# Optimization experiments

Hardware: AMD Instinct MI355X
Metric: run time of the kernel (lower is better)

Reference implementation:

```python
import jax, jax.numpy as jnp
import numpy as np

B, S, D, F, H, R, BLK = 1, 2048, 1024, 2816, 16, 16, 64
DH = D // H  # 64

# bitsandbytes NF4 codebook
NF4_CODE = jnp.array([-1.0, -0.6961928009986877, -0.5250730514526367, -0.39491748809814453,
                      -0.28444138169288635, -0.18477343022823334, -0.09105003625154495, 0.0,
                      0.07958029955625534, 0.16093020141124725, 0.24611230194568634, 0.33791524171829224,
                      0.44070982933044434, 0.5626170039176941, 0.7229568362236023, 1.0], dtype=jnp.float32)


def dequant_nf4(codes, absmax, shape):
    # blockwise NF4 dequant: codebook lookup * per-64-element absmax scale
    w = NF4_CODE[codes.reshape(-1)]
    return (w.reshape(-1, BLK) * absmax[:, None]).reshape(shape)


def rmsnorm(x, w, eps=1e-10):
    return x * jax.lax.rsqrt(jnp.mean(x * x, axis=-1, keepdims=True) + eps) * w


def rotate_half(x):
    x1, x2 = jnp.split(x, 2, axis=-1)
    return jnp.concatenate((-x2, x1), axis=-1)


def apply_rope(x, cos, sin, pos):
    # x: [B,H,S,DH], pos: [B,S] -> gather rope tables per position
    c = cos[pos][:, None]  # [B,1,S,DH]
    s = sin[pos][:, None]
    return x * c + rotate_half(x) * s


def proj(x, codes, absmax, la, lb, shape):
    # fused NF4 dequant-matmul + additive LoRA branch: x @ W.T + (x @ A) @ B
    w = dequant_nf4(codes, absmax, shape)
    return x @ w.T + (x @ la) @ lb


def _forward(x, nw1, nw2, cos, sin,
             qa, qla, qlb, ka, kla, klb, va, vla, vlb, oa, ola, olb,
             ga, gla, glb, ua, ula, ulb, da, dla, dlb,
             pos, qc, kc, vc, oc, gc, uc, dc):
    h1 = rmsnorm(x, nw1)
    q = proj(h1, qc, qa, qla, qlb, (D, D))
    k = proj(h1, kc, ka, kla, klb, (D, D))
    v = proj(h1, vc, va, vla, vlb, (D, D))

    def heads(t):
        return t.reshape(B, S, H, DH).transpose(0, 2, 1, 3)

    q = apply_rope(heads(q), cos, sin, pos)
    k = apply_rope(heads(k), cos, sin, pos)
    v = heads(v)

    scores = jnp.einsum('bhqd,bhkd->bhqk', q, k) / np.float32(np.sqrt(DH))
    causal = jnp.tril(jnp.ones((S, S), dtype=bool))
    mask = jnp.where(causal, 0.0, -1e9).astype(scores.dtype)  # additive attention_mask
    attn = jax.nn.softmax(scores + mask, axis=-1)
    o = jnp.einsum('bhqk,bhkd->bhqd', attn, v).transpose(0, 2, 1, 3).reshape(B, S, D)
    o = proj(o, oc, oa, ola, olb, (D, D))

    x1 = x + o  # first residual
    h2 = rmsnorm(x1, nw2)
    gate = proj(h2, gc, ga, gla, glb, (F, D))
    up = proj(h2, uc, ua, ula, ulb, (F, D))
    had = up * jax.nn.silu(gate)  # SwiGLU hadamard
    down = proj(had, dc, da, dla, dlb, (D, F))
    return x1 + down


def setup_inputs():
    ks = iter(jax.random.split(jax.random.key(0), 48))

    def rn(shape, scale=1.0):
        return jax.random.normal(next(ks), shape, jnp.float32) * scale

    def cd(shape):
        return jax.random.randint(next(ks), shape, 0, 16, dtype=jnp.int32)

    def am(n):
        return jax.random.uniform(next(ks), (n,), jnp.float32) * 0.04 + 0.01

    inp = {'x': rn((B, S, D)),
           'norm_weight_1': 1.0 + rn((D,), 0.02),
           'norm_weight_2': 1.0 + rn((D,), 0.02)}
    inv = 1.0 / (10000.0 ** (jnp.arange(0, DH, 2, dtype=jnp.float32) / DH))
    ang = jnp.arange(S, dtype=jnp.float32)[:, None] * inv[None, :]
    emb = jnp.concatenate((ang, ang), axis=-1)  # [S, DH]
    inp['cos'], inp['sin'] = jnp.cos(emb), jnp.sin(emb)
    inp['position_ids'] = jnp.broadcast_to(jnp.arange(S, dtype=jnp.int32), (B, S))
    shapes = {'q': (D, D), 'k': (D, D), 'v': (D, D), 'o': (D, D),
              'gate': (F, D), 'up': (F, D), 'down': (D, F)}
    for p, (o, i) in shapes.items():
        inp['w_%s_codes' % p] = cd((o, i))
        inp['w_%s_absmax' % p] = am(o * i // BLK)
        inp['w_%s_lora_a' % p] = rn((i, R), 1.0 / np.sqrt(i))
        inp['w_%s_lora_b' % p] = rn((R, o), 0.01)
    return inp


def reference(x, norm_weight_1, norm_weight_2, cos, sin, position_ids,
              w_q_codes, w_q_absmax, w_q_lora_a, w_q_lora_b,
              w_k_codes, w_k_absmax, w_k_lora_a, w_k_lora_b,
              w_v_codes, w_v_absmax, w_v_lora_a, w_v_lora_b,
              w_o_codes, w_o_absmax, w_o_lora_a, w_o_lora_b,
              w_gate_codes, w_gate_absmax, w_gate_lora_a, w_gate_lora_b,
              w_up_codes, w_up_absmax, w_up_lora_a, w_up_lora_b,
              w_down_codes, w_down_absmax, w_down_lora_a, w_down_lora_b):
    return _forward(x, norm_weight_1, norm_weight_2, cos, sin,
                    w_q_absmax, w_q_lora_a, w_q_lora_b,
                    w_k_absmax, w_k_lora_a, w_k_lora_b,
                    w_v_absmax, w_v_lora_a, w_v_lora_b,
                    w_o_absmax, w_o_lora_a, w_o_lora_b,
                    w_gate_absmax, w_gate_lora_a, w_gate_lora_b,
                    w_up_absmax, w_up_lora_a, w_up_lora_b,
                    w_down_absmax, w_down_lora_a, w_down_lora_b,
                    position_ids, w_q_codes, w_k_codes, w_v_codes,
                    w_o_codes, w_gate_codes, w_up_codes, w_down_codes)
```

## Files before the change

### kernel.cpp

```cpp
#include <hip/hip_runtime.h>
#include <stdint.h>


#define Sq   2048
#define Dm   1024
#define Fm   2816
#define Hh   16
#define KE1  1088
#define KE2  1056
#define KE3  2848
#define NQKV 3072
#define NGU  5632

typedef short bf16x8 __attribute__((ext_vector_type(8)));
typedef float f32x4  __attribute__((ext_vector_type(4)));

__constant__ float NF4_LUT[16] = {
    -1.0f, -0.6961928009986877f, -0.5250730514526367f, -0.39491748809814453f,
    -0.28444138169288635f, -0.18477343022823334f, -0.09105003625154495f, 0.0f,
    0.07958029955625534f, 0.16093020141124725f, 0.24611230194568634f,
    0.33791524171829224f, 0.44070982933044434f, 0.5626170039176941f,
    0.7229568362236023f, 1.0f};

__device__ inline unsigned short f2bf(float f) {
    union { float f; uint32_t u; } v; v.f = f;
    uint32_t u = v.u;
    return (unsigned short)((u + 0x7FFFu + ((u >> 16) & 1u)) >> 16);
}
__device__ inline float bf2f(unsigned short h) {
    union { uint32_t u; float f; } v; v.u = ((uint32_t)h) << 16;
    return v.f;
}
__device__ inline unsigned short truncbf(float f) {
    union { float f; uint32_t u; } v; v.f = f;
    return (unsigned short)(v.u >> 16);
}

#define GLD16(gp, lp)                                                         \
    __builtin_amdgcn_global_load_lds(                                         \
        (__attribute__((address_space(1))) void*)(uintptr_t)(gp),             \
        (__attribute__((address_space(3))) void*)(uint32_t)(uintptr_t)(lp),   \
        16, 0, 0)

__global__ __launch_bounds__(256) void rmsnorm_ext(
    const float* __restrict__ X, const float* __restrict__ W,
    unsigned short* Hout, int ldh)
{
    int s = blockIdx.x, tid = threadIdx.x;
    const float4 v = *(const float4*)(X + (size_t)s * Dm + tid * 4);
    float ss = v.x * v.x + v.y * v.y + v.z * v.z + v.w * v.w;
#pragma unroll
    for (int m = 1; m < 64; m <<= 1) ss += __shfl_xor(ss, m);
    __shared__ float red[4];
    int lane = tid & 63, wave = tid >> 6;
    if (lane == 0) red[wave] = ss;
    __syncthreads();
    float scale = rsqrtf((red[0] + red[1] + red[2] + red[3]) * (1.0f / Dm) + 1e-10f);
    const float4 w = *(const float4*)(W + tid * 4);
    alignas(8) unsigned short o[4];
    o[0] = f2bf(v.x * scale * w.x);
    o[1] = f2bf(v.y * scale * w.y);
    o[2] = f2bf(v.z * scale * w.z);
    o[3] = f2bf(v.w * scale * w.w);
    *(ushort4*)(Hout + (size_t)s * ldh + tid * 4) = *(ushort4*)o;
    if (tid < 64) Hout[(size_t)s * ldh + Dm + tid] = 0;
}

__global__ __launch_bounds__(256) void lora_prep(
    const float* __restrict__ qla, const float* __restrict__ kla,
    const float* __restrict__ vla, const float* __restrict__ ola,
    const float* __restrict__ gla, const float* __restrict__ ula,
    const float* __restrict__ dla, unsigned short* __restrict__ lapk)
{
    int tid = threadIdx.x;
    int chunk = blockIdx.x * 4 + (tid >> 6);
    int lane = tid & 63;
    int lr = lane & 15, quad = lane >> 4;
    const float* la;
    int lc;
    if (chunk < 192) {
        int m = chunk >> 5; lc = chunk & 31;
        la = (m == 0) ? qla : (m == 1) ? kla : (m == 2) ? vla
           : (m == 3) ? ola : (m == 4) ? gla : ula;
    } else {
        la = dla; lc = chunk - 192;
    }
    alignas(16) unsigned short out[8];
#pragma unroll
    for (int e = 0; e < 8; ++e)
        out[e] = f2bf(la[(size_t)(lc * 32 + quad * 8 + e) * 16 + lr]);
    *(uint4*)(lapk + (size_t)chunk * 512 + lane * 8) = *(uint4*)out;
}

template<int NM>
__global__ __launch_bounds__(256) void lora_mfma(
    unsigned short* Aext, int lda, int K,
    const unsigned short* __restrict__ lapk, int c0, int c1, int c2,
    int toff, int zoff, int zn)
{
    int tid = threadIdx.x;
    int lane = tid & 63, wave = tid >> 6;
    int lr = lane & 15, quad = lane >> 4;
    int r0 = blockIdx.x * 16;
    int nc4 = K >> 7;
    int gc0 = wave * nc4;
    const unsigned short* Ab = Aext + (size_t)(r0 + lr) * lda + quad * 8;
    int cb[3] = {c0, c1, c2};
    f32x4 zero = {0.f, 0.f, 0.f, 0.f};
    f32x4 acc[NM];
#pragma unroll
    for (int m = 0; m < NM; ++m) acc[m] = zero;
    for (int cc = 0; cc < nc4; ++cc) {
        int gc = gc0 + cc;
        bf16x8 af = *(const bf16x8*)(Ab + gc * 32);
#pragma unroll
        for (int m = 0; m < NM; ++m) {
            bf16x8 bf = *(const bf16x8*)(lapk + (size_t)(cb[m] + gc) * 512 + lane * 8);
            acc[m] = __builtin_amdgcn_mfma_f32_16x16x32_bf16(af, bf, acc[m], 0, 0, 0);
        }
    }
    __shared__ float red[3][NM * 64 * 4];
    if (wave > 0) {
#pragma unroll
        for (int m = 0; m < NM; ++m)
#pragma unroll
            for (int r = 0; r < 4; ++r)
                red[wave - 1][(m * 64 + lane) * 4 + r] = acc[m][r];
    }
    __syncthreads();
    if (wave == 0) {
#pragma unroll
        for (int m = 0; m < NM; ++m)
#pragma unroll
            for (int r = 0; r < 4; ++r)
                acc[m][r] += red[0][(m * 64 + lane) * 4 + r]
                           + red[1][(m * 64 + lane) * 4 + r]
                           + red[2][(m * 64 + lane) * 4 + r];
#pragma unroll
        for (int r = 0; r < 4; ++r) {
            int row = r0 + quad * 4 + r;
#pragma unroll
            for (int m = 0; m < NM; ++m)
                Aext[(size_t)row * lda + toff + m * 16 + lr] = f2bf(acc[m][r]);
        }
        if (zn > 0) {
            int row = r0 + lr, j0 = quad * 4;
            if (j0 < zn) {
                alignas(8) unsigned short z4[4] = {0, 0, 0, 0};
                *(ushort4*)(Aext + (size_t)row * lda + zoff + j0) = *(ushort4*)z4;
            }
        }
    }
}

__device__ inline void dq_row8(const float* lut, const int* cod, const float* am,
                               const float* lb, int nr, int c8, int K, int Nlb,
                               int toff, unsigned short* out)
{
    if (c8 < K) {
        size_t base = (size_t)nr * K + c8;
        const int4* cp = (const int4*)(cod + base);
        int4 ca = cp[0], cb = cp[1];
        float a = am[base >> 6];
        out[0] = f2bf(lut[ca.x] * a); out[1] = f2bf(lut[ca.y] * a);
        out[2] = f2bf(lut[ca.z] * a); out[3] = f2bf(lut[ca.w] * a);
        out[4] = f2bf(lut[cb.x] * a); out[5] = f2bf(lut[cb.y] * a);
        out[6] = f2bf(lut[cb.z] * a); out[7] = f2bf(lut[cb.w] * a);
    } else {
        int r = c8 - toff;
#pragma unroll
        for (int i = 0; i < 8; ++i) out[i] = 0;
        if (r >= 0 && r < 16) {
#pragma unroll
            for (int i = 0; i < 8; ++i) out[i] = f2bf(lb[(size_t)(r + i) * Nlb + nr]);
        }
    }
}

__global__ __launch_bounds__(256) void dequant_qkv(
    const int* __restrict__ qc, const int* __restrict__ kc, const int* __restrict__ vc,
    const float* __restrict__ qa, const float* __restrict__ ka, const float* __restrict__ va,
    const float* __restrict__ qlb, const float* __restrict__ klb, const float* __restrict__ vlb,
    unsigned short* __restrict__ Wout)
{
    __shared__ float lut[16];
    if (threadIdx.x < 16) lut[threadIdx.x] = NF4_LUT[threadIdx.x];
    __syncthreads();
    int idx = blockIdx.x * 256 + threadIdx.x;
    int n = idx / 136;
    int c8 = (idx - n * 136) * 8;
    int seg = n >> 10, nr = n & 1023;
    const int* cod   = (seg == 0) ? qc : (seg == 1) ? kc : vc;
    const float* am  = (seg == 0) ? qa : (seg == 1) ? ka : va;
    const float* lb  = (seg == 0) ? qlb : (seg == 1) ? klb : vlb;
    int toff = 1024 + (seg << 4);
    alignas(16) unsigned short out[8];
    dq_row8(lut, cod, am, lb, nr, c8, 1024, 1024, toff, out);
    *(uint4*)(Wout + (size_t)n * KE1 + c8) = *(uint4*)out;
}

__global__ __launch_bounds__(256) void dequant_gu(
    const int* __restrict__ gc, const int* __restrict__ uc,
    const float* __restrict__ ga, const float* __restrict__ ua,
    const float* __restrict__ glb, const float* __restrict__ ulb,
    unsigned short* __restrict__ Wout)
{
    __shared__ float lut[16];
    if (threadIdx.x < 16) lut[threadIdx.x] = NF4_LUT[threadIdx.x];
    __syncthreads();
    int idx = blockIdx.x * 256 + threadIdx.x;
    int n = idx / 132;
    int c8 = (idx - n * 132) * 8;
    int m = n >> 1, mat = n & 1;
    const int* cod  = mat ? uc : gc;
    const float* am = mat ? ua : ga;
    const float* lb = mat ? ulb : glb;
    int toff = 1024 + (mat << 4);
    alignas(16) unsigned short out[8];
    dq_row8(lut, cod, am, lb, m, c8, 1024, Fm, toff, out);
    *(uint4*)(Wout + (size_t)n * KE2 + c8) = *(uint4*)out;
}

__global__ __launch_bounds__(256) void dequant_ext(
    const int* __restrict__ codes, const float* __restrict__ absmax,
    const float* __restrict__ lb, unsigned short* __restrict__ Wout,
    int Nproj, int K, int ldw, int toff)
{
    __shared__ float lut[16];
    if (threadIdx.x < 16) lut[threadIdx.x] = NF4_LUT[threadIdx.x];
    __syncthreads();
    int idx = blockIdx.x * 256 + threadIdx.x;
    int cpr = ldw >> 3;
    int n = idx / cpr;
    if (n >= Nproj) return;
    int c8 = (idx - n * cpr) * 8;
    alignas(16) unsigned short out[8];
    dq_row8(lut, codes, absmax, lb, n, c8, K, Nproj, toff, out);
    *(uint4*)(Wout + (size_t)n * ldw + c8) = *(uint4*)out;
}

__global__ __launch_bounds__(256) void gemm128(
    const unsigned short* __restrict__ A, int lda,
    const unsigned short* __restrict__ B, int ldb, int K,
    unsigned short* __restrict__ Cb, int ldc)
{
    __shared__ __align__(16) unsigned short At[2][128 * 32];
    __shared__ __align__(16) unsigned short Bt[2][128 * 32];
    int tid = threadIdx.x;
    int lane = tid & 63, wave = tid >> 6;
    int lr = lane & 15, quad = lane >> 4;
    int wm = (wave >> 1) * 64, wn = (wave & 1) * 64;
    int row0 = blockIdx.x * 128, col0 = blockIdx.y * 128;
    f32x4 acc[4][4];
    f32x4 zero = {0.f, 0.f, 0.f, 0.f};
#pragma unroll
    for (int i = 0; i < 4; ++i)
#pragma unroll
        for (int j = 0; j < 4; ++j) acc[i][j] = zero;
    int sw = ((tid & 3) ^ ((tid >> 3) & 3)) * 8;
    const unsigned short* Ag  = A + (size_t)(row0 + (tid >> 2)) * lda + sw;
    const unsigned short* Ag2 = Ag + (size_t)64 * lda;
    const unsigned short* Bg  = B + (size_t)(col0 + (tid >> 2)) * ldb + sw;
    const unsigned short* Bg2 = Bg + (size_t)64 * ldb;
    int l0 = tid * 8, l1 = (tid + 256) * 8;
    GLD16(Ag, At[0] + l0); GLD16(Ag2, At[0] + l1);
    GLD16(Bg, Bt[0] + l0); GLD16(Bg2, Bt[0] + l1);
    int sq = (quad ^ ((lr >> 1) & 3)) * 8;
    int nIter = K >> 5;
    for (int it = 0; it < nIter; ++it) {
        int cur = it & 1;
        __syncthreads();
        if (it + 1 < nIter) {
            int k = (it + 1) << 5, nx = cur ^ 1;
            GLD16(Ag + k, At[nx] + l0); GLD16(Ag2 + k, At[nx] + l1);
            GLD16(Bg + k, Bt[nx] + l0); GLD16(Bg2 + k, Bt[nx] + l1);
        }
        bf16x8 af[4], bfr[4];
#pragma unroll
        for (int i = 0; i < 4; ++i)
            af[i] = *(const bf16x8*)(At[cur] + (wm + i * 16 + lr) * 32 + sq);
#pragma unroll
        for (int j = 0; j < 4; ++j)
            bfr[j] = *(const bf16x8*)(Bt[cur] + (wn + j * 16 + lr) * 32 + sq);
#pragma unroll
        for (int i = 0; i < 4; ++i)
#pragma unroll
            for (int j = 0; j < 4; ++j)
                acc[i][j] = __builtin_amdgcn_mfma_f32_16x16x32_bf16(af[i], bfr[j], acc[i][j], 0, 0, 0);
    }
#pragma unroll
    for (int i = 0; i < 4; ++i) {
        int rowb = row0 + wm + i * 16 + quad * 4;
#pragma unroll
        for (int j = 0; j < 4; ++j) {
            int col = col0 + wn + j * 16 + lr;
#pragma unroll
            for (int r = 0; r < 4; ++r)
                Cb[(size_t)(rowb + r) * ldc + col] = f2bf(acc[i][j][r]);
        }
    }
}

__global__ __launch_bounds__(256) void gemm_gu(
    const unsigned short* __restrict__ A, int lda,
    const unsigned short* __restrict__ B, int ldb, int K,
    unsigned short* __restrict__ Hb)
{
    __shared__ __align__(16) unsigned short At[2][128 * 32];
    __shared__ __align__(16) unsigned short Bt[2][128 * 32];
    int tid = threadIdx.x;
    int lane = tid & 63, wave = tid >> 6;
    int lr = lane & 15, quad = lane >> 4;
    int wm = (wave >> 1) * 64, wn = (wave & 1) * 64;
    int row0 = blockIdx.x * 128, col0 = blockIdx.y * 128;
    f32x4 acc[4][4];
    f32x4 zero = {0.f, 0.f, 0.f, 0.f};
#pragma unroll
    for (int i = 0; i < 4; ++i)
#pragma unroll
        for (int j = 0; j < 4; ++j) acc[i][j] = zero;
    int sw = ((tid & 3) ^ ((tid >> 3) & 3)) * 8;
    const unsigned short* Ag  = A + (size_t)(row0 + (tid >> 2)) * lda + sw;
    const unsigned short* Ag2 = Ag + (size_t)64 * lda;
    const unsigned short* Bg  = B + (size_t)(col0 + (tid >> 2)) * ldb + sw;
    const unsigned short* Bg2 = Bg + (size_t)64 * ldb;
    int l0 = tid * 8, l1 = (tid + 256) * 8;
    GLD16(Ag, At[0] + l0); GLD16(Ag2, At[0] + l1);
    GLD16(Bg, Bt[0] + l0); GLD16(Bg2, Bt[0] + l1);
    int sq = (quad ^ ((lr >> 1) & 3)) * 8;
    int nIter = K >> 5;
    for (int it = 0; it < nIter; ++it) {
        int cur = it & 1;
        __syncthreads();
        if (it + 1 < nIter) {
            int k = (it + 1) << 5, nx = cur ^ 1;
            GLD16(Ag + k, At[nx] + l0); GLD16(Ag2 + k, At[nx] + l1);
            GLD16(Bg + k, Bt[nx] + l0); GLD16(Bg2 + k, Bt[nx] + l1);
        }
        bf16x8 af[4], bfr[4];
#pragma unroll
        for (int i = 0; i < 4; ++i)
            af[i] = *(const bf16x8*)(At[cur] + (wm + i * 16 + lr) * 32 + sq);
#pragma unroll
        for (int j = 0; j < 4; ++j)
            bfr[j] = *(const bf16x8*)(Bt[cur] + (wn + j * 16 + lr) * 32 + sq);
#pragma unroll
        for (int i = 0; i < 4; ++i)
#pragma unroll
            for (int j = 0; j < 4; ++j)
                acc[i][j] = __builtin_amdgcn_mfma_f32_16x16x32_bf16(af[i], bfr[j], acc[i][j], 0, 0, 0);
    }
#pragma unroll
    for (int i = 0; i < 4; ++i) {
        int rowb = row0 + wm + i * 16 + quad * 4;
#pragma unroll
        for (int j = 0; j < 4; ++j) {
            int col = col0 + wn + j * 16 + lr;
#pragma unroll
            for (int r = 0; r < 4; ++r) {
                float own = acc[i][j][r];
                float oth = __shfl_xor(own, 1);
                if (!(lr & 1)) {
                    float sig = 1.0f / (1.0f + __expf(-own));
                    Hb[(size_t)(rowb + r) * KE3 + (col >> 1)] = f2bf(oth * own * sig);
                }
            }
        }
    }
}

template<int TAG>
__global__ __launch_bounds__(256) void gemm_s(
    const unsigned short* __restrict__ A, int lda,
    const unsigned short* __restrict__ B, int ldb, int K,
    float* __restrict__ Cf, int ldc, const float* __restrict__ Radd)
{
    __shared__ __align__(16) unsigned short At[2][64 * 32];
    __shared__ __align__(16) unsigned short Bt[2][64 * 32];
    int tid = threadIdx.x;
    int lane = tid & 63, wave = tid >> 6;
    int lr = lane & 15, quad = lane >> 4;
    int row0 = blockIdx.x * 64, col0 = blockIdx.y * 64;
    f32x4 acc[4];
    f32x4 zero = {0.f, 0.f, 0.f, 0.f};
#pragma unroll
    for (int j = 0; j < 4; ++j) acc[j] = zero;
    int sw = ((tid & 3) ^ ((tid >> 3) & 3)) * 8;
    const unsigned short* Ag = A + (size_t)(row0 + (tid >> 2)) * lda + sw;
    const unsigned short* Bg = B + (size_t)(col0 + (tid >> 2)) * ldb + sw;
    int l0 = tid * 8;
    GLD16(Ag, At[0] + l0);
    GLD16(Bg, Bt[0] + l0);
    int sq = (quad ^ ((lr >> 1) & 3)) * 8;
    int nIter = K >> 5;
    for (int it = 0; it < nIter; ++it) {
        int cur = it & 1;
        __syncthreads();
        if (it + 1 < nIter) {
            int k = (it + 1) << 5, nx = cur ^ 1;
            GLD16(Ag + k, At[nx] + l0);
            GLD16(Bg + k, Bt[nx] + l0);
        }
        bf16x8 af = *(const bf16x8*)(At[cur] + (wave * 16 + lr) * 32 + sq);
        bf16x8 bfr[4];
#pragma unroll
        for (int j = 0; j < 4; ++j)
            bfr[j] = *(const bf16x8*)(Bt[cur] + (j * 16 + lr) * 32 + sq);
#pragma unroll
        for (int j = 0; j < 4; ++j)
            acc[j] = __builtin_amdgcn_mfma_f32_16x16x32_bf16(af, bfr[j], acc[j], 0, 0, 0);
    }
    int rowb = row0 + wave * 16 + quad * 4;
#pragma unroll
    for (int j = 0; j < 4; ++j) {
        int col = col0 + j * 16 + lr;
#pragma unroll
        for (int r = 0; r < 4; ++r) {
            size_t o = (size_t)(rowb + r) * ldc + col;
            Cf[o] = acc[j][r] + Radd[o];
        }
    }
}

__global__ __launch_bounds__(256) void rope_pack(
    const unsigned short* __restrict__ qkv,
    const float* __restrict__ cosT, const float* __restrict__ sinT,
    const int* __restrict__ pos,
    unsigned short* __restrict__ qb, unsigned short* __restrict__ kpk,
    unsigned short* __restrict__ vpk)
{
    int b = blockIdx.x, tid = threadIdx.x;
    if (b < 8192) {
        int idx = b * 256 + tid;
        int s = idx >> 10, col = idx & 1023, d = col & 63;
        int p = pos[s];
        float c = cosT[p * 64 + d], sn = sinT[p * 64 + d];
        int partner = (d < 32) ? (col + 32) : (col - 32);
        float sgn = (d < 32) ? -1.f : 1.f;
        const unsigned short* row = qkv + (size_t)s * NQKV;
        float q = bf2f(row[col]), q2 = bf2f(row[partner]);
        qb[idx] = f2bf((q * c + sgn * q2 * sn) * 0.125f);
    } else if (b < 9216) {
        int g = (b - 8192) * 256 + tid;
        int lr = g & 15, quad = (g >> 4) & 3, cch = (g >> 6) & 1;
        int t = (g >> 7) & 127, h = g >> 14;
        int s = t * 16 + lr;
        int p = pos[s];
        int d0 = cch * 32 + quad * 8;
        const unsigned short* krow = qkv + (size_t)s * NQKV + Dm + h * 64;
        uint4 kv8 = *(const uint4*)(krow + d0);
        uint4 kp8 = *(const uint4*)(krow + ((d0 + 32) & 63));
        float sgn = (d0 < 32) ? -1.f : 1.f;
        const float* cp = cosT + p * 64 + d0;
        const float* sp = sinT + p * 64 + d0;
        const unsigned short* ke = (const unsigned short*)&kv8;
        const unsigned short* pe = (const unsigned short*)&kp8;
        alignas(16) unsigned short out[8];
#pragma unroll
        for (int e = 0; e < 8; ++e)
            out[e] = f2bf(bf2f(ke[e]) * cp[e] + sgn * bf2f(pe[e]) * sp[e]);
        *(uint4*)(kpk + (size_t)g * 8) = *(uint4*)out;
    } else {
        int g = (b - 9216) * 256 + tid;
        int lrr = g & 15, quad = (g >> 4) & 3, kk = (g >> 6) & 3;
        int j = (g >> 8) & 3, kt = (g >> 10) & 15, h = g >> 14;
        int d = j * 16 + lrr;
        int sbase = kt * 128 + kk * 32 + quad * 8;
        alignas(16) unsigned short out[8];
#pragma unroll
        for (int e = 0; e < 8; ++e)
            out[e] = qkv[(size_t)(sbase + e) * NQKV + 2048 + h * 64 + d];
        *(uint4*)(vpk + (size_t)g * 8) = *(uint4*)out;
    }
}

__global__ __launch_bounds__(256) void attn(
    const unsigned short* __restrict__ qb, const unsigned short* __restrict__ kpk,
    const unsigned short* __restrict__ vpk, unsigned short* __restrict__ ob)
{
    __shared__ __align__(16) unsigned short Ps[4][16 * 136];
    int tid = threadIdx.x;
    int lane = tid & 63, wave = tid >> 6;
    int lr = lane & 15, quad = lane >> 4;
    int idx = blockIdx.x;
    int t_ = idx >> 4;
    int qt = (idx < 256) ? (31 - t_) : (t_ - 16);
    int h = idx & 15;
    int r0 = qt * 64 + wave * 16;
    const unsigned short* qp = qb + (size_t)(r0 + lr) * Dm + h * 64 + quad * 8;
    bf16x8 qf0 = *(const bf16x8*)qp;
    bf16x8 qf1 = *(const bf16x8*)(qp + 32);
    const unsigned short* kpb = kpk + (size_t)h * 128 * 1024 + lane * 8;
    const unsigned short* vpb = vpk + (size_t)h * 16 * 16 * 512 + lane * 8;
    f32x4 zero = {0.f, 0.f, 0.f, 0.f};
    f32x4 oacc[4];
#pragma unroll
    for (int j = 0; j < 4; ++j) oacc[j] = zero;
    float lrow[4] = {0.f, 0.f, 0.f, 0.f};
    int ntile = (qt * 64 + 191) >> 7;

    for (int kt = 0; kt < ntile; ++kt) {
        int k0 = kt << 7;
        f32x4 sf[8];
#pragma unroll
        for (int jj = 0; jj < 8; ++jj) {
            const unsigned short* kp = kpb + (size_t)(kt * 8 + jj) * 1024;
            bf16x8 kf0 = *(const bf16x8*)kp;
            bf16x8 kf1 = *(const bf16x8*)(kp + 512);
            f32x4 z = zero;
            z = __builtin_amdgcn_mfma_f32_16x16x32_bf16(qf0, kf0, z, 0, 0, 0);
            z = __builtin_amdgcn_mfma_f32_16x16x32_bf16(qf1, kf1, z, 0, 0, 0);
            sf[jj] = z;
        }
        bf16x8 vf[4][4];
#pragma unroll
        for (int j = 0; j < 4; ++j)
#pragma unroll
            for (int kk = 0; kk < 4; ++kk)
                vf[j][kk] = *(const bf16x8*)(vpb + (size_t)((kt * 4 + j) * 4 + kk) * 512);
        if (kt == ntile - 1) {
#pragma unroll
            for (int jj = 0; jj < 8; ++jj)
#pragma unroll
                for (int r = 0; r < 4; ++r)
                    if (k0 + jj * 16 + lr > r0 + quad * 4 + r)
                        sf[jj][r] = -1e30f;
        }
#pragma unroll
        for (int jj = 0; jj < 8; ++jj)
#pragma unroll
            for (int r = 0; r < 4; ++r) {
                float p = __expf(sf[jj][r]);
                sf[jj][r] = p;
                lrow[r] += p;
            }
#pragma unroll
        for (int jj = 0; jj < 8; ++jj)
#pragma unroll
            for (int r = 0; r < 4; ++r)
                Ps[wave][(quad * 4 + r) * 136 + jj * 16 + lr] = truncbf(sf[jj][r]);
        bf16x8 pf[4];
#pragma unroll
        for (int kk = 0; kk < 4; ++kk)
            pf[kk] = *(const bf16x8*)(&Ps[wave][lr * 136 + kk * 32 + quad * 8]);
#pragma unroll
        for (int j = 0; j < 4; ++j)
#pragma unroll
            for (int kk = 0; kk < 4; ++kk)
                oacc[j] = __builtin_amdgcn_mfma_f32_16x16x32_bf16(pf[kk], vf[j][kk], oacc[j], 0, 0, 0);
    }
#pragma unroll
    for (int r = 0; r < 4; ++r)
#pragma unroll
        for (int m = 1; m < 16; m <<= 1) lrow[r] += __shfl_xor(lrow[r], m);
#pragma unroll
    for (int r = 0; r < 4; ++r) {
        float inv = 1.0f / lrow[r];
        int row = r0 + quad * 4 + r;
#pragma unroll
        for (int j = 0; j < 4; ++j)
            ob[(size_t)row * KE2 + h * 64 + j * 16 + lr] = f2bf(oacc[j][r] * inv);
    }
}

extern "C" void kernel_launch(void* const* d_in, const int* in_sizes, int n_in,
                              void* d_out, int out_size, void* d_ws, size_t ws_size,
                              hipStream_t stream)
{
    const float* x    = (const float*)d_in[0];
    const float* nw1  = (const float*)d_in[1];
    const float* nw2  = (const float*)d_in[2];
    const float* cosT = (const float*)d_in[3];
    const float* sinT = (const float*)d_in[4];
    const int*   pos  = (const int*)d_in[5];
    const int   *qc = (const int*)d_in[6],  *kc = (const int*)d_in[10],
                *vc = (const int*)d_in[14], *oc = (const int*)d_in[18],
                *gc = (const int*)d_in[22], *uc = (const int*)d_in[26],
                *dc = (const int*)d_in[30];
    const float *qa = (const float*)d_in[7],  *ka = (const float*)d_in[11],
                *va = (const float*)d_in[15], *oa = (const float*)d_in[19],
                *ga = (const float*)d_in[23], *ua = (const float*)d_in[27],
                *da = (const float*)d_in[31];
    const float *qla = (const float*)d_in[8],  *kla = (const float*)d_in[12],
                *vla = (const float*)d_in[16], *ola = (const float*)d_in[20],
                *gla = (const float*)d_in[24], *ula = (const float*)d_in[28],
                *dla = (const float*)d_in[32];
    const float *qlb = (const float*)d_in[9],  *klb = (const float*)d_in[13],
                *vlb = (const float*)d_in[17], *olb = (const float*)d_in[21],
                *glb = (const float*)d_in[25], *ulb = (const float*)d_in[29],
                *dlb = (const float*)d_in[33];

    char* ws = (char*)d_ws;
    unsigned short* h     = (unsigned short*)(ws + 0);
    unsigned short* W     = (unsigned short*)(ws + 4456448);
    unsigned short* qkv   = (unsigned short*)(ws + 16351232);
    unsigned short* lapkB = (unsigned short*)(ws + 16351232);
    unsigned short* qbf   = (unsigned short*)(ws + 28934144);
    unsigned short* kpk   = (unsigned short*)(ws + 33128448);
    unsigned short* vpk   = (unsigned short*)(ws + 37322752);
    unsigned short* obf   = (unsigned short*)(ws + 41517056);
    unsigned short* lapkA = (unsigned short*)(ws + 41517056);
    float*          x1    = (float*)(ws + 45842432);
    unsigned short* hb    = (unsigned short*)(ws + 54231040);
    float* outp = (float*)d_out;

    lora_prep<<<70, 256, 0, stream>>>(qla, kla, vla, ola, gla, ula, dla, lapkA);
    rmsnorm_ext<<<Sq, 256, 0, stream>>>(x, nw1, h, KE1);
    lora_mfma<3><<<128, 256, 0, stream>>>(h, KE1, Dm, lapkA, 0, 32, 64, 1024, 0, 0);
    dequant_qkv<<<1632, 256, 0, stream>>>(qc, kc, vc, qa, ka, va, qlb, klb, vlb, W);
    gemm128<<<dim3(Sq / 128, NQKV / 128), 256, 0, stream>>>(h, KE1, W, KE1, KE1, qkv, NQKV);
    rope_pack<<<10240, 256, 0, stream>>>(qkv, cosT, sinT, pos, qbf, kpk, vpk);
    lora_prep<<<70, 256, 0, stream>>>(qla, kla, vla, ola, gla, ula, dla, lapkB);
    attn<<<512, 256, 0, stream>>>(qbf, kpk, vpk, obf);
    lora_mfma<1><<<128, 256, 0, stream>>>(obf, KE2, Dm, lapkB, 96, 0, 0, 1024, 1040, 16);
    dequant_ext<<<528, 256, 0, stream>>>(oc, oa, olb, W, Dm, Dm, KE2, 1024);
    gemm_s<0><<<dim3(Sq / 64, Dm / 64), 256, 0, stream>>>(obf, KE2, W, KE2, KE2, x1, Dm, x);
    rmsnorm_ext<<<Sq, 256, 0, stream>>>(x1, nw2, h, KE1);
    lora_mfma<2><<<128, 256, 0, stream>>>(h, KE1, Dm, lapkB, 128, 160, 0, 1024, 0, 0);
    dequant_gu<<<2904, 256, 0, stream>>>(gc, uc, ga, ua, glb, ulb, W);
    gemm_gu<<<dim3(Sq / 128, NGU / 128), 256, 0, stream>>>(h, KE1, W, KE2, KE2, hb);
    lora_mfma<1><<<128, 256, 0, stream>>>(hb, KE3, Fm, lapkB, 192, 0, 0, 2816, 2832, 16);
    dequant_ext<<<1424, 256, 0, stream>>>(dc, da, dlb, W, Dm, Fm, KE3, 2816);
    gemm_s<1><<<dim3(Sq / 64, Dm / 64), 256, 0, stream>>>(hb, KE3, W, KE3, KE3, outp, Dm, x1);
}
```

Measured before the change: 371.6 us.

## Use K=64 tiles in small GEMM, swap grid order, reorganize workspace

The small-tile output GEMMs now stage 64-wide K slices with an 8-way XOR swizzle and issue two MFMAs per stage, halving the number of barriers and loop iterations. The extended K dimensions are padded to multiples of 64 (KE2 1088, KE3 2880), and the dequant grids grow to match. All GEMM grids now map blockIdx.x to output columns, so consecutive blocks share A rows for better L2 reuse. The workspace is repacked so the LoRA pack is prepared once, which removes the second lora_prep launch; the padding adds some extra zero-K work.

```diff
diff --git a/kernel.cpp b/kernel.cpp
--- a/kernel.cpp
+++ b/kernel.cpp
@@ -7,8 +7,8 @@
 #define Fm   2816
 #define Hh   16
 #define KE1  1088
-#define KE2  1056
-#define KE3  2848
+#define KE2  1088
+#define KE3  2880
 #define NQKV 3072
 #define NGU  5632
 
@@ -209,8 +209,8 @@
     if (threadIdx.x < 16) lut[threadIdx.x] = NF4_LUT[threadIdx.x];
     __syncthreads();
     int idx = blockIdx.x * 256 + threadIdx.x;
-    int n = idx / 132;
-    int c8 = (idx - n * 132) * 8;
+    int n = idx / 136;
+    int c8 = (idx - n * 136) * 8;
     int m = n >> 1, mat = n & 1;
     const int* cod  = mat ? uc : gc;
     const float* am = mat ? ua : ga;
@@ -250,7 +250,7 @@
     int lane = tid & 63, wave = tid >> 6;
     int lr = lane & 15, quad = lane >> 4;
     int wm = (wave >> 1) * 64, wn = (wave & 1) * 64;
-    int row0 = blockIdx.x * 128, col0 = blockIdx.y * 128;
+    int row0 = blockIdx.y * 128, col0 = blockIdx.x * 128;
     f32x4 acc[4][4];
     f32x4 zero = {0.f, 0.f, 0.f, 0.f};
 #pragma unroll
@@ -312,7 +312,7 @@
     int lane = tid & 63, wave = tid >> 6;
     int lr = lane & 15, quad = lane >> 4;
     int wm = (wave >> 1) * 64, wn = (wave & 1) * 64;
-    int row0 = blockIdx.x * 128, col0 = blockIdx.y * 128;
+    int row0 = blockIdx.y * 128, col0 = blockIdx.x * 128;
     f32x4 acc[4][4];
     f32x4 zero = {0.f, 0.f, 0.f, 0.f};
 #pragma unroll
@@ -375,40 +375,51 @@
     const unsigned short* __restrict__ B, int ldb, int K,
     float* __restrict__ Cf, int ldc, const float* __restrict__ Radd)
 {
-    __shared__ __align__(16) unsigned short At[2][64 * 32];
-    __shared__ __align__(16) unsigned short Bt[2][64 * 32];
+    __shared__ __align__(16) unsigned short At[2][64 * 64];
+    __shared__ __align__(16) unsigned short Bt[2][64 * 64];
     int tid = threadIdx.x;
     int lane = tid & 63, wave = tid >> 6;
     int lr = lane & 15, quad = lane >> 4;
-    int row0 = blockIdx.x * 64, col0 = blockIdx.y * 64;
+    int row0 = blockIdx.y * 64, col0 = blockIdx.x * 64;
     f32x4 acc[4];
     f32x4 zero = {0.f, 0.f, 0.f, 0.f};
 #pragma unroll
     for (int j = 0; j < 4; ++j) acc[j] = zero;
-    int sw = ((tid & 3) ^ ((tid >> 3) & 3)) * 8;
-    const unsigned short* Ag = A + (size_t)(row0 + (tid >> 2)) * lda + sw;
-    const unsigned short* Bg = B + (size_t)(col0 + (tid >> 2)) * ldb + sw;
-    int l0 = tid * 8;
-    GLD16(Ag, At[0] + l0);
-    GLD16(Bg, Bt[0] + l0);
-    int sq = (quad ^ ((lr >> 1) & 3)) * 8;
-    int nIter = K >> 5;
+    int rs = tid >> 3;
+    int g8 = ((tid & 7) ^ (rs & 7)) * 8;
+    const unsigned short* Ag  = A + (size_t)(row0 + rs) * lda + g8;
+    const unsigned short* Ag2 = Ag + (size_t)32 * lda;
+    const unsigned short* Bg  = B + (size_t)(col0 + rs) * ldb + g8;
+    const unsigned short* Bg2 = Bg + (size_t)32 * ldb;
+    int l0 = tid * 8, l1 = (tid + 256) * 8;
+    GLD16(Ag, At[0] + l0); GLD16(Ag2, At[0] + l1);
+    GLD16(Bg, Bt[0] + l0); GLD16(Bg2, Bt[0] + l1);
+    int c0 = (quad ^ (lr & 7)) * 8;
+    int c1 = ((4 + quad) ^ (lr & 7)) * 8;
+    int nIter = K >> 6;
     for (int it = 0; it < nIter; ++it) {
         int cur = it & 1;
         __syncthreads();
         if (it + 1 < nIter) {
-            int k = (it + 1) << 5, nx = cur ^ 1;
-            GLD16(Ag + k, At[nx] + l0);
-            GLD16(Bg + k, Bt[nx] + l0);
-        }
-        bf16x8 af = *(const bf16x8*)(At[cur] + (wave * 16 + lr) * 32 + sq);
-        bf16x8 bfr[4];
-#pragma unroll
-        for (int j = 0; j < 4; ++j)
-            bfr[j] = *(const bf16x8*)(Bt[cur] + (j * 16 + lr) * 32 + sq);
-#pragma unroll
-        for (int j = 0; j < 4; ++j)
-            acc[j] = __builtin_amdgcn_mfma_f32_16x16x32_bf16(af, bfr[j], acc[j], 0, 0, 0);
+            int k = (it + 1) << 6, nx = cur ^ 1;
+            GLD16(Ag + k, At[nx] + l0); GLD16(Ag2 + k, At[nx] + l1);
+            GLD16(Bg + k, Bt[nx] + l0); GLD16(Bg2 + k, Bt[nx] + l1);
+        }
+        const unsigned short* arow = At[cur] + (wave * 16 + lr) * 64;
+        bf16x8 a0 = *(const bf16x8*)(arow + c0);
+        bf16x8 a1 = *(const bf16x8*)(arow + c1);
+        bf16x8 b0[4], b1[4];
+#pragma unroll
+        for (int j = 0; j < 4; ++j) {
+            const unsigned short* brow = Bt[cur] + (j * 16 + lr) * 64;
+            b0[j] = *(const bf16x8*)(brow + c0);
+            b1[j] = *(const bf16x8*)(brow + c1);
+        }
+#pragma unroll
+        for (int j = 0; j < 4; ++j) {
+            acc[j] = __builtin_amdgcn_mfma_f32_16x16x32_bf16(a0, b0[j], acc[j], 0, 0, 0);
+            acc[j] = __builtin_amdgcn_mfma_f32_16x16x32_bf16(a1, b1[j], acc[j], 0, 0, 0);
+        }
     }
     int rowb = row0 + wave * 16 + quad * 4;
 #pragma unroll
@@ -591,35 +602,33 @@
                 *dlb = (const float*)d_in[33];
 
     char* ws = (char*)d_ws;
-    unsigned short* h     = (unsigned short*)(ws + 0);
-    unsigned short* W     = (unsigned short*)(ws + 4456448);
-    unsigned short* qkv   = (unsigned short*)(ws + 16351232);
-    unsigned short* lapkB = (unsigned short*)(ws + 16351232);
-    unsigned short* qbf   = (unsigned short*)(ws + 28934144);
-    unsigned short* kpk   = (unsigned short*)(ws + 33128448);
-    unsigned short* vpk   = (unsigned short*)(ws + 37322752);
-    unsigned short* obf   = (unsigned short*)(ws + 41517056);
-    unsigned short* lapkA = (unsigned short*)(ws + 41517056);
-    float*          x1    = (float*)(ws + 45842432);
-    unsigned short* hb    = (unsigned short*)(ws + 54231040);
+    unsigned short* h    = (unsigned short*)(ws + 0);
+    unsigned short* W    = (unsigned short*)(ws + 4456448);
+    unsigned short* qkv  = (unsigned short*)(ws + 16711680);
+    unsigned short* qbf  = (unsigned short*)(ws + 29294592);
+    unsigned short* kpk  = (unsigned short*)(ws + 33488896);
+    unsigned short* vpk  = (unsigned short*)(ws + 37683200);
+    unsigned short* obf  = (unsigned short*)(ws + 41877504);
+    float*          x1   = (float*)(ws + 29294592);
+    unsigned short* hb   = (unsigned short*)(ws + 46333952);
+    unsigned short* lapk = (unsigned short*)(ws + 58130432);
     float* outp = (float*)d_out;
 
-    lora_prep<<<70, 256, 0, stream>>>(qla, kla, vla, ola, gla, ula, dla, lapkA);
+    lora_prep<<<70, 256, 0, stream>>>(qla, kla, vla, ola, gla, ula, dla, lapk);
     rmsnorm_ext<<<Sq, 256, 0, stream>>>(x, nw1, h, KE1);
-    lora_mfma<3><<<128, 256, 0, stream>>>(h, KE1, Dm, lapkA, 0, 32, 64, 1024, 0, 0);
+    lora_mfma<3><<<128, 256, 0, stream>>>(h, KE1, Dm, lapk, 0, 32, 64, 1024, 0, 0);
     dequant_qkv<<<1632, 256, 0, stream>>>(qc, kc, vc, qa, ka, va, qlb, klb, vlb, W);
-    gemm128<<<dim3(Sq / 128, NQKV / 128), 256, 0, stream>>>(h, KE1, W, KE1, KE1, qkv, NQKV);
+    gemm128<<<dim3(NQKV / 128, Sq / 128), 256, 0, stream>>>(h, KE1, W, KE1, KE1, qkv, NQKV);
     rope_pack<<<10240, 256, 0, stream>>>(qkv, cosT, sinT, pos, qbf, kpk, vpk);
-    lora_prep<<<70, 256, 0, stream>>>(qla, kla, vla, ola, gla, ula, dla, lapkB);
     attn<<<512, 256, 0, stream>>>(qbf, kpk, vpk, obf);
-    lora_mfma<1><<<128, 256, 0, stream>>>(obf, KE2, Dm, lapkB, 96, 0, 0, 1024, 1040, 16);
-    dequant_ext<<<528, 256, 0, stream>>>(oc, oa, olb, W, Dm, Dm, KE2, 1024);
-    gemm_s<0><<<dim3(Sq / 64, Dm / 64), 256, 0, stream>>>(obf, KE2, W, KE2, KE2, x1, Dm, x);
+    lora_mfma<1><<<128, 256, 0, stream>>>(obf, KE2, Dm, lapk, 96, 0, 0, 1024, 1040, 16);
+    dequant_ext<<<544, 256, 0, stream>>>(oc, oa, olb, W, Dm, Dm, KE2, 1024);
+    gemm_s<0><<<dim3(Dm / 64, Sq / 64), 256, 0, stream>>>(obf, KE2, W, KE2, KE2, x1, Dm, x);
     rmsnorm_ext<<<Sq, 256, 0, stream>>>(x1, nw2, h, KE1);
-    lora_mfma<2><<<128, 256, 0, stream>>>(h, KE1, Dm, lapkB, 128, 160, 0, 1024, 0, 0);
-    dequant_gu<<<2904, 256, 0, stream>>>(gc, uc, ga, ua, glb, ulb, W);
-    gemm_gu<<<dim3(Sq / 128, NGU / 128), 256, 0, stream>>>(h, KE1, W, KE2, KE2, hb);
-    lora_mfma<1><<<128, 256, 0, stream>>>(hb, KE3, Fm, lapkB, 192, 0, 0, 2816, 2832, 16);
-    dequant_ext<<<1424, 256, 0, stream>>>(dc, da, dlb, W, Dm, Fm, KE3, 2816);
-    gemm_s<1><<<dim3(Sq / 64, Dm / 64), 256, 0, stream>>>(hb, KE3, W, KE3, KE3, outp, Dm, x1);
-}
+    lora_mfma<2><<<128, 256, 0, stream>>>(h, KE1, Dm, lapk, 128, 160, 0, 1024, 0, 0);
+    dequant_gu<<<2992, 256, 0, stream>>>(gc, uc, ga, ua, glb, ulb, W);
+    gemm_gu<<<dim3(NGU / 128, Sq / 128), 256, 0, stream>>>(h, KE1, W, KE2, KE2, hb);
+    lora_mfma<1><<<128, 256, 0, stream>>>(hb, KE3, Fm, lapk, 192, 0, 0, 2816, 2832, 16);
+    dequant_ext<<<1440, 256, 0, stream>>>(dc, da, dlb, W, Dm, Fm, KE3, 2816);
+    gemm_s<1><<<dim3(Dm / 64, Sq / 64), 256, 0, stream>>>(hb, KE3, W, KE3, KE3, outp, Dm, x1);
+}
```

Result: faster. 346.8 us (-6.7%).
